# Kernel optimization log

Measured on AMD Instinct MI355X. Metric: run time of the kernel, lower is better.

## Reference

```python
import jax, jax.numpy as jnp
import numpy as np


def setup_inputs() -> dict:
    key = jax.random.key(0)
    k1, k2, k3 = jax.random.split(key, 3)
    B, T = 4096, 8192
    X = jax.random.normal(k1, (B, T), dtype=jnp.float32)
    raw_a = jax.random.normal(k2, (), dtype=jnp.float32)
    raw_b = jax.random.normal(k3, (), dtype=jnp.float32)
    return {"X": X, "raw_a": raw_a, "raw_b": raw_b}


def reference(X, raw_a, raw_b):
    # project: a = 0.5*tanh(raw_a); per-step input u_t = a * x_t
    # forward step: z_t = u_t + b * z_{t-1},  b = tanh(raw_b),  z_0 = 0
    # readout: squeeze the size-1 hidden dim (already scalar here)
    a = 0.5 * jnp.tanh(raw_a)
    b = jnp.tanh(raw_b)
    u = a * X                      # [B, T]
    mult = jnp.full_like(u, b)     # constant decay per step

    # Affine composition: (m1, s1) then (m2, s2) -> (m2*m1, m2*s1 + s2)
    def combine(c1, c2):
        m1, s1 = c1
        m2, s2 = c2
        return (m1 * m2, m2 * s1 + s2)

    _, Z = jax.lax.associative_scan(combine, (mult, u), axis=1)
    return Z  # [B, T] hidden states over all timesteps
```

## Files before the change

kernel.cpp:

```cpp
#include <hip/hip_runtime.h>
#include <math.h>


typedef float f32x4 __attribute__((ext_vector_type(4)));

#define T_LEN  8192
#define NSUB   4
#define CHUNK  1024
#define NCHUNK (T_LEN / CHUNK)

__global__ __launch_bounds__(256) void lincell_scan(
    const float* __restrict__ X,
    const float* __restrict__ pa,
    const float* __restrict__ pb,
    float* __restrict__ Z,
    int nrows)
{
    const int gtid = blockIdx.x * blockDim.x + threadIdx.x;
    const int row  = gtid >> 6;
    const int lane = threadIdx.x & 63;
    if (row >= nrows) return;

    const float a  = 0.5f * tanhf(pa[0]);
    const float b  = tanhf(pb[0]);
    const float b2 = b * b;
    const float b3 = b2 * b;
    const float b4 = b2 * b2;

    float mstep[6];
#pragma unroll
    for (int k = 0; k < 6; ++k) {
        const int d = 1 << k;
        const int e = (lane + 1 < d) ? (lane + 1) : d;
        mstep[k] = powf(b4, (float)e);
    }
    const float b4lane = powf(b4, (float)lane);
    const float bsub   = powf(b4, 64.0f);

    const f32x4* xrow = (const f32x4*)(X + (size_t)row * T_LEN);
    f32x4*       zrow = (f32x4*)(Z + (size_t)row * T_LEN);

    float carry = 0.0f;

    f32x4 cur[NSUB];
#pragma unroll
    for (int j = 0; j < NSUB; ++j) cur[j] = xrow[j * 64 + lane];

#pragma unroll
    for (int c = 0; c < NCHUNK; ++c) {
        f32x4 nxt[NSUB];
        if (c + 1 < NCHUNK) {
#pragma unroll
            for (int j = 0; j < NSUB; ++j)
                nxt[j] = xrow[(c + 1) * 256 + j * 64 + lane];
        }

        float y0[NSUB], y1[NSUB], y2[NSUB], y3[NSUB], s[NSUB];
#pragma unroll
        for (int j = 0; j < NSUB; ++j) {
            y0[j] = a * cur[j].x;
            y1[j] = fmaf(b, y0[j], a * cur[j].y);
            y2[j] = fmaf(b, y1[j], a * cur[j].z);
            y3[j] = fmaf(b, y2[j], a * cur[j].w);
            s[j]  = y3[j];
        }

#pragma unroll
        for (int k = 0; k < 6; ++k) {
#pragma unroll
            for (int j = 0; j < NSUB; ++j) {
                float t = __shfl_up(s[j], (unsigned)(1 << k), 64);
                t = (lane >= (1 << k)) ? t : 0.0f;
                s[j] = fmaf(mstep[k], t, s[j]);
            }
        }

        float excl[NSUB], tot[NSUB];
#pragma unroll
        for (int j = 0; j < NSUB; ++j) {
            float e = __shfl_up(s[j], 1u, 64);
            excl[j] = (lane >= 1) ? e : 0.0f;
            tot[j]  = __shfl(s[j], 63, 64);
        }

        float cj = carry;
#pragma unroll
        for (int j = 0; j < NSUB; ++j) {
            const float pre = fmaf(b4lane, cj, excl[j]);
            f32x4 o;
            o.x = fmaf(b,  pre, y0[j]);
            o.y = fmaf(b2, pre, y1[j]);
            o.z = fmaf(b3, pre, y2[j]);
            o.w = fmaf(b4, pre, y3[j]);
            __builtin_nontemporal_store(o, &zrow[c * 256 + j * 64 + lane]);
            cj = fmaf(bsub, cj, tot[j]);
        }
        carry = cj;

#pragma unroll
        for (int j = 0; j < NSUB; ++j) cur[j] = nxt[j];
    }
}

extern "C" void kernel_launch(void* const* d_in, const int* in_sizes, int n_in,
                              void* d_out, int out_size, void* d_ws, size_t ws_size,
                              hipStream_t stream) {
    const float* X  = (const float*)d_in[0];
    const float* pa = (const float*)d_in[1];
    const float* pb = (const float*)d_in[2];
    float* Z = (float*)d_out;

    const int nrows = in_sizes[0] / T_LEN;
    const int blocks = (nrows + 3) / 4;
    lincell_scan<<<blocks, 256, 0, stream>>>(X, pa, pb, Z, nrows);
}
```

Measured before the change: 236.0 us.

## Scan each row with a 1024-thread block using a two-level wave scan

Switches from one wavefront per row walking eight sequential chunks to one 1024-thread block per row. Each of the 16 waves scans 512 elements, and the wave totals are combined through shared memory by a 16-wide scan in wave 0. This removes the serial chunk carry chain and the per-wave register-heavy prefetch. In exchange it adds two block barriers and recomputes powf for the cross-wave decay factors, and each thread now issues only one round of loads before it must wait.

```diff
diff --git a/kernel.cpp b/kernel.cpp
--- a/kernel.cpp
+++ b/kernel.cpp
@@ -4,21 +4,22 @@
 
 typedef float f32x4 __attribute__((ext_vector_type(4)));
 
-#define T_LEN  8192
-#define NSUB   4
-#define CHUNK  1024
-#define NCHUNK (T_LEN / CHUNK)
+#define T_LEN 8192
 
-__global__ __launch_bounds__(256) void lincell_scan(
+__global__ __launch_bounds__(1024) void lincell_scan(
     const float* __restrict__ X,
     const float* __restrict__ pa,
     const float* __restrict__ pb,
     float* __restrict__ Z,
     int nrows)
 {
-    const int gtid = blockIdx.x * blockDim.x + threadIdx.x;
-    const int row  = gtid >> 6;
-    const int lane = threadIdx.x & 63;
+    __shared__ float wsum[16];
+    __shared__ float wcarry[16];
+
+    const int row  = blockIdx.x;
+    const int tid  = threadIdx.x;
+    const int wave = tid >> 6;
+    const int lane = tid & 63;
     if (row >= nrows) return;
 
     const float a  = 0.5f * tanhf(pa[0]);
@@ -35,71 +36,85 @@
         mstep[k] = powf(b4, (float)e);
     }
     const float b4lane = powf(b4, (float)lane);
-    const float bsub   = powf(b4, 64.0f);
+    const float b256   = powf(b4, 64.0f);
+    const float b512   = b256 * b256;
 
     const f32x4* xrow = (const f32x4*)(X + (size_t)row * T_LEN);
     f32x4*       zrow = (f32x4*)(Z + (size_t)row * T_LEN);
 
-    float carry = 0.0f;
+    const int base = wave * 128 + lane;
+    const f32x4 v0 = xrow[base];
+    const f32x4 v1 = xrow[base + 64];
 
-    f32x4 cur[NSUB];
-#pragma unroll
-    for (int j = 0; j < NSUB; ++j) cur[j] = xrow[j * 64 + lane];
+    float y0[2], y1[2], y2[2], y3[2], s[2];
+    y0[0] = a * v0.x;
+    y1[0] = fmaf(b, y0[0], a * v0.y);
+    y2[0] = fmaf(b, y1[0], a * v0.z);
+    y3[0] = fmaf(b, y2[0], a * v0.w);
+    y0[1] = a * v1.x;
+    y1[1] = fmaf(b, y0[1], a * v1.y);
+    y2[1] = fmaf(b, y1[1], a * v1.z);
+    y3[1] = fmaf(b, y2[1], a * v1.w);
+    s[0] = y3[0];
+    s[1] = y3[1];
 
 #pragma unroll
-    for (int c = 0; c < NCHUNK; ++c) {
-        f32x4 nxt[NSUB];
-        if (c + 1 < NCHUNK) {
+    for (int k = 0; k < 6; ++k) {
 #pragma unroll
-            for (int j = 0; j < NSUB; ++j)
-                nxt[j] = xrow[(c + 1) * 256 + j * 64 + lane];
+        for (int j = 0; j < 2; ++j) {
+            float t = __shfl_up(s[j], (unsigned)(1 << k), 64);
+            t = (lane >= (1 << k)) ? t : 0.0f;
+            s[j] = fmaf(mstep[k], t, s[j]);
         }
+    }
+    float excl[2], tot[2];
+#pragma unroll
+    for (int j = 0; j < 2; ++j) {
+        float e = __shfl_up(s[j], 1u, 64);
+        excl[j] = (lane >= 1) ? e : 0.0f;
+        tot[j]  = __shfl(s[j], 63, 64);
+    }
 
-        float y0[NSUB], y1[NSUB], y2[NSUB], y3[NSUB], s[NSUB];
+    const float Wt = fmaf(b256, tot[0], tot[1]);
+    if (lane == 0) wsum[wave] = Wt;
+    __syncthreads();
+
+    if (wave == 0) {
+        float s16 = (lane < 16) ? wsum[lane] : 0.0f;
 #pragma unroll
-        for (int j = 0; j < NSUB; ++j) {
-            y0[j] = a * cur[j].x;
-            y1[j] = fmaf(b, y0[j], a * cur[j].y);
-            y2[j] = fmaf(b, y1[j], a * cur[j].z);
-            y3[j] = fmaf(b, y2[j], a * cur[j].w);
-            s[j]  = y3[j];
+        for (int k = 0; k < 4; ++k) {
+            const int d = 1 << k;
+            const int e = (lane + 1 < d) ? (lane + 1) : d;
+            const float m16 = powf(b512, (float)e);
+            float t = __shfl_up(s16, (unsigned)d, 64);
+            t = (lane >= d) ? t : 0.0f;
+            s16 = fmaf(m16, t, s16);
         }
+        float e16 = __shfl_up(s16, 1u, 64);
+        e16 = (lane >= 1) ? e16 : 0.0f;
+        if (lane < 16) wcarry[lane] = e16;
+    }
+    __syncthreads();
 
-#pragma unroll
-        for (int k = 0; k < 6; ++k) {
-#pragma unroll
-            for (int j = 0; j < NSUB; ++j) {
-                float t = __shfl_up(s[j], (unsigned)(1 << k), 64);
-                t = (lane >= (1 << k)) ? t : 0.0f;
-                s[j] = fmaf(mstep[k], t, s[j]);
-            }
-        }
+    const float carry = wcarry[wave];
+    const float c0 = carry;
+    const float c1 = fmaf(b256, carry, tot[0]);
 
-        float excl[NSUB], tot[NSUB];
-#pragma unroll
-        for (int j = 0; j < NSUB; ++j) {
-            float e = __shfl_up(s[j], 1u, 64);
-            excl[j] = (lane >= 1) ? e : 0.0f;
-            tot[j]  = __shfl(s[j], 63, 64);
-        }
+    const float pre0 = fmaf(b4lane, c0, excl[0]);
+    const float pre1 = fmaf(b4lane, c1, excl[1]);
 
-        float cj = carry;
-#pragma unroll
-        for (int j = 0; j < NSUB; ++j) {
-            const float pre = fmaf(b4lane, cj, excl[j]);
-            f32x4 o;
-            o.x = fmaf(b,  pre, y0[j]);
-            o.y = fmaf(b2, pre, y1[j]);
-            o.z = fmaf(b3, pre, y2[j]);
-            o.w = fmaf(b4, pre, y3[j]);
-            __builtin_nontemporal_store(o, &zrow[c * 256 + j * 64 + lane]);
-            cj = fmaf(bsub, cj, tot[j]);
-        }
-        carry = cj;
+    f32x4 o0, o1;
+    o0.x = fmaf(b,  pre0, y0[0]);
+    o0.y = fmaf(b2, pre0, y1[0]);
+    o0.z = fmaf(b3, pre0, y2[0]);
+    o0.w = fmaf(b4, pre0, y3[0]);
+    o1.x = fmaf(b,  pre1, y0[1]);
+    o1.y = fmaf(b2, pre1, y1[1]);
+    o1.z = fmaf(b3, pre1, y2[1]);
+    o1.w = fmaf(b4, pre1, y3[1]);
 
-#pragma unroll
-        for (int j = 0; j < NSUB; ++j) cur[j] = nxt[j];
-    }
+    __builtin_nontemporal_store(o0, &zrow[base]);
+    __builtin_nontemporal_store(o1, &zrow[base + 64]);
 }
 
 extern "C" void kernel_launch(void* const* d_in, const int* in_sizes, int n_in,
@@ -111,6 +126,5 @@
     float* Z = (float*)d_out;
 
     const int nrows = in_sizes[0] / T_LEN;
-    const int blocks = (nrows + 3) / 4;
-    lincell_scan<<<blocks, 256, 0, stream>>>(X, pa, pb, Z, nrows);
+    lincell_scan<<<nrows, 1024, 0, stream>>>(X, pa, pb, Z, nrows);
 }
```

New measurement: 286.6 us. +21.4%, slower.

## Split each row across four waves with shared-memory carry combine

Applied to the files above, without the earlier changes.

Each row is now handled by a 256-thread block, so each wave scans a 2048-element segment in one shot instead of one wave walking eight sequential chunks. Wave totals are exchanged through shared memory and combined with a b^2048 decay to form per-wave carries. The aim is more waves and more outstanding memory loads to hide latency on a bandwidth-bound scan. The cost is higher register use per thread and a block-wide barrier. The powf-based decay powers are also replaced with repeated squaring.

```diff
diff --git a/kernel.cpp b/kernel.cpp
--- a/kernel.cpp
+++ b/kernel.cpp
@@ -4,10 +4,8 @@
 
 typedef float f32x4 __attribute__((ext_vector_type(4)));
 
-#define T_LEN  8192
-#define NSUB   4
-#define CHUNK  1024
-#define NCHUNK (T_LEN / CHUNK)
+#define T_LEN 8192
+#define NSUB  8
 
 __global__ __launch_bounds__(256) void lincell_scan(
     const float* __restrict__ X,
@@ -16,9 +14,12 @@
     float* __restrict__ Z,
     int nrows)
 {
-    const int gtid = blockIdx.x * blockDim.x + threadIdx.x;
-    const int row  = gtid >> 6;
-    const int lane = threadIdx.x & 63;
+    __shared__ float wsum[4];
+
+    const int row  = blockIdx.x;
+    const int tid  = threadIdx.x;
+    const int wave = tid >> 6;
+    const int lane = tid & 63;
     if (row >= nrows) return;
 
     const float a  = 0.5f * tanhf(pa[0]);
@@ -27,78 +28,81 @@
     const float b3 = b2 * b;
     const float b4 = b2 * b2;
 
-    float mstep[6];
-#pragma unroll
-    for (int k = 0; k < 6; ++k) {
-        const int d = 1 << k;
-        const int e = (lane + 1 < d) ? (lane + 1) : d;
-        mstep[k] = powf(b4, (float)e);
-    }
-    const float b4lane = powf(b4, (float)lane);
-    const float bsub   = powf(b4, 64.0f);
+    const float m1  = b4;
+    const float m2  = m1  * m1;
+    const float m4  = m2  * m2;
+    const float m8  = m4  * m4;
+    const float m16 = m8  * m8;
+    const float m32 = m16 * m16;
+    const float b256  = m32 * m32;
+    const float b2048 = b256 * b256 * b256 * b256 * b256 * b256 * b256 * b256;
+    const float mstep[6] = { m1, m2, m4, m8, m16, m32 };
+
+    float b4lane = 1.0f;
+    b4lane *= (lane & 1)  ? m1  : 1.0f;
+    b4lane *= (lane & 2)  ? m2  : 1.0f;
+    b4lane *= (lane & 4)  ? m4  : 1.0f;
+    b4lane *= (lane & 8)  ? m8  : 1.0f;
+    b4lane *= (lane & 16) ? m16 : 1.0f;
+    b4lane *= (lane & 32) ? m32 : 1.0f;
 
     const f32x4* xrow = (const f32x4*)(X + (size_t)row * T_LEN);
     f32x4*       zrow = (f32x4*)(Z + (size_t)row * T_LEN);
 
-    float carry = 0.0f;
+    const int vbase = wave * 512 + lane;
+    f32x4 v[NSUB];
+#pragma unroll
+    for (int j = 0; j < NSUB; ++j) v[j] = xrow[vbase + j * 64];
 
-    f32x4 cur[NSUB];
+    float y0[NSUB], y1[NSUB], y2[NSUB], y3[NSUB], s[NSUB];
 #pragma unroll
-    for (int j = 0; j < NSUB; ++j) cur[j] = xrow[j * 64 + lane];
+    for (int j = 0; j < NSUB; ++j) {
+        y0[j] = a * v[j].x;
+        y1[j] = fmaf(b, y0[j], a * v[j].y);
+        y2[j] = fmaf(b, y1[j], a * v[j].z);
+        y3[j] = fmaf(b, y2[j], a * v[j].w);
+        s[j]  = y3[j];
+    }
 
 #pragma unroll
-    for (int c = 0; c < NCHUNK; ++c) {
-        f32x4 nxt[NSUB];
-        if (c + 1 < NCHUNK) {
-#pragma unroll
-            for (int j = 0; j < NSUB; ++j)
-                nxt[j] = xrow[(c + 1) * 256 + j * 64 + lane];
-        }
-
-        float y0[NSUB], y1[NSUB], y2[NSUB], y3[NSUB], s[NSUB];
+    for (int k = 0; k < 6; ++k) {
 #pragma unroll
         for (int j = 0; j < NSUB; ++j) {
-            y0[j] = a * cur[j].x;
-            y1[j] = fmaf(b, y0[j], a * cur[j].y);
-            y2[j] = fmaf(b, y1[j], a * cur[j].z);
-            y3[j] = fmaf(b, y2[j], a * cur[j].w);
-            s[j]  = y3[j];
+            float t = __shfl_up(s[j], (unsigned)(1 << k), 64);
+            t = (lane >= (1 << k)) ? t : 0.0f;
+            s[j] = fmaf(mstep[k], t, s[j]);
         }
+    }
+    float excl[NSUB], tot[NSUB];
+#pragma unroll
+    for (int j = 0; j < NSUB; ++j) {
+        float e = __shfl_up(s[j], 1u, 64);
+        excl[j] = (lane >= 1) ? e : 0.0f;
+        tot[j]  = __shfl(s[j], 63, 64);
+    }
 
+    float Wt = tot[0];
 #pragma unroll
-        for (int k = 0; k < 6; ++k) {
+    for (int j = 1; j < NSUB; ++j) Wt = fmaf(b256, Wt, tot[j]);
+    if (lane == 0) wsum[wave] = Wt;
+    __syncthreads();
+
+    float carry = 0.0f;
+    if (wave > 0) carry = wsum[0];
+    if (wave > 1) carry = fmaf(b2048, carry, wsum[1]);
+    if (wave > 2) carry = fmaf(b2048, carry, wsum[2]);
+
+    float cj = carry;
 #pragma unroll
-            for (int j = 0; j < NSUB; ++j) {
-                float t = __shfl_up(s[j], (unsigned)(1 << k), 64);
-                t = (lane >= (1 << k)) ? t : 0.0f;
-                s[j] = fmaf(mstep[k], t, s[j]);
-            }
-        }
-
-        float excl[NSUB], tot[NSUB];
-#pragma unroll
-        for (int j = 0; j < NSUB; ++j) {
-            float e = __shfl_up(s[j], 1u, 64);
-            excl[j] = (lane >= 1) ? e : 0.0f;
-            tot[j]  = __shfl(s[j], 63, 64);
-        }
-
-        float cj = carry;
-#pragma unroll
-        for (int j = 0; j < NSUB; ++j) {
-            const float pre = fmaf(b4lane, cj, excl[j]);
-            f32x4 o;
-            o.x = fmaf(b,  pre, y0[j]);
-            o.y = fmaf(b2, pre, y1[j]);
-            o.z = fmaf(b3, pre, y2[j]);
-            o.w = fmaf(b4, pre, y3[j]);
-            __builtin_nontemporal_store(o, &zrow[c * 256 + j * 64 + lane]);
-            cj = fmaf(bsub, cj, tot[j]);
-        }
-        carry = cj;
-
-#pragma unroll
-        for (int j = 0; j < NSUB; ++j) cur[j] = nxt[j];
+    for (int j = 0; j < NSUB; ++j) {
+        const float pre = fmaf(b4lane, cj, excl[j]);
+        f32x4 o;
+        o.x = fmaf(b,  pre, y0[j]);
+        o.y = fmaf(b2, pre, y1[j]);
+        o.z = fmaf(b3, pre, y2[j]);
+        o.w = fmaf(b4, pre, y3[j]);
+        __builtin_nontemporal_store(o, &zrow[vbase + j * 64]);
+        cj = fmaf(b256, cj, tot[j]);
     }
 }
 
@@ -111,6 +115,5 @@
     float* Z = (float*)d_out;
 
     const int nrows = in_sizes[0] / T_LEN;
-    const int blocks = (nrows + 3) / 4;
-    lincell_scan<<<blocks, 256, 0, stream>>>(X, pa, pb, Z, nrows);
+    lincell_scan<<<nrows, 256, 0, stream>>>(X, pa, pb, Z, nrows);
 }
```

Measured after the change: 239.2 us. No clear change (+1.3%).
